# Kernel tuning notes

Measured on AMD Instinct MI355X. Metric: run time of the kernel, lower is better.

## Reference

```python
import jax, jax.numpy as jnp
import numpy as np

ROTATION_SHIFT = 15
B, L = 4096, 2048  # batch, code length


def _shift_schedule(r):
    # [0, -1, 1, -2, 2, ..., -r, r] as in the torch loop
    s = [0]
    for x in range(1, r + 1):
        s += [-x, x]
    return jnp.asarray(s, dtype=jnp.int32)


def setup_inputs() -> dict:
    key = jax.random.key(0)
    k1, k2, k3, k4 = jax.random.split(key, 4)
    shape = (2, B, L, 2)
    mk = lambda k: jax.random.randint(k, shape, 0, 2).astype(jnp.bool_)
    return {
        "iris_codes_a": mk(k1),
        "mask_codes_a": mk(k2),
        "iris_codes_b": mk(k3),
        "mask_codes_b": mk(k4),
    }


def reference(iris_codes_a, mask_codes_a, iris_codes_b, mask_codes_b):
    shifts = _shift_schedule(ROTATION_SHIFT)

    def hdist(shift):
        # roll probe codes along the code-length axis (axis=2 of (2,B,L,2))
        ia = jnp.roll(iris_codes_a, shift, axis=2)
        ma = jnp.roll(mask_codes_a, shift, axis=2)
        maskbits = ma & mask_codes_b                      # (2,B,L,2) bool
        irisbits = (ia != iris_codes_b) & maskbits        # masked non-matching bits
        # counts can exceed 2^24, so accumulate in int32 before casting
        num = jnp.sum(irisbits, dtype=jnp.int32).astype(jnp.float32)
        den = jnp.sum(maskbits, dtype=jnp.int32).astype(jnp.float32)
        return num / den

    init = jnp.minimum(jnp.ones((), jnp.float32), hdist(shifts[0]))

    def step(carry, s):
        return jnp.minimum(carry, hdist(s)), None

    match_dist, _ = jax.lax.scan(step, init, shifts[1:])
    return match_dist.reshape(1)  # torch.ones(1) makes the output shape (1,)
```

## Files before the change

### kernel.cpp

```cpp
#include <hip/hip_runtime.h>
#include <stdint.h>

typedef unsigned long long u64;
typedef unsigned int u32;

#define NACC    31
#define NSHIFT  15
#define NROWS   8192
#define ROWB    4096
#define NBLK    2048
#define NSHADOW 32

__device__ __forceinline__ void pack16(uint4 v, u32& P0, u32& P1, int t) {
    const u32 q0 = __byte_perm(v.x, v.y, 0x6420);
    const u32 q1 = __byte_perm(v.x, v.y, 0x7531);
    const u32 q2 = __byte_perm(v.z, v.w, 0x6420);
    const u32 q3 = __byte_perm(v.z, v.w, 0x7531);
    const u32 n0 = (q0 * 0x01020408u) >> 24;
    const u32 n1 = (q1 * 0x01020408u) >> 24;
    const u32 n2 = (q2 * 0x01020408u) >> 24;
    const u32 n3 = (q3 * 0x01020408u) >> 24;
    P0 |= (n0 | (n2 << 4)) << (8 * t);
    P1 |= (n1 | (n3 << 4)) << (8 * t);
}

__global__ __launch_bounds__(256) void hd_main(
    const unsigned char* __restrict__ ia, const unsigned char* __restrict__ ma,
    const unsigned char* __restrict__ ib, const unsigned char* __restrict__ mb,
    u32* __restrict__ cnt)
{
    const int tid  = threadIdx.x;
    const int lane = tid & 63;
    const int row  = blockIdx.x * 4 + (tid >> 6);

    u32 acc[NACC];
#pragma unroll
    for (int j = 0; j < NACC; ++j) acc[j] = 0u;

    const int prevL = (lane + 63) & 63;
    const int nextL = (lane + 1) & 63;

    {
        const uint4* pa = (const uint4*)(ia + (size_t)row * ROWB) + lane * 4;
        const uint4* pm = (const uint4*)(ma + (size_t)row * ROWB) + lane * 4;
        const uint4* pb = (const uint4*)(ib + (size_t)row * ROWB) + lane * 4;
        const uint4* pn = (const uint4*)(mb + (size_t)row * ROWB) + lane * 4;

        u32 A0 = 0, A1 = 0, M0 = 0, M1 = 0, B0 = 0, B1 = 0, N0 = 0, N1 = 0;
#pragma unroll
        for (int t = 0; t < 4; ++t) {
            const uint4 va = pa[t];
            const uint4 vm = pm[t];
            const uint4 vb = pb[t];
            const uint4 vn = pn[t];
            pack16(va, A0, A1, t);
            pack16(vm, M0, M1, t);
            pack16(vb, B0, B1, t);
            pack16(vn, N0, N1, t);
        }

        const u32 pA0 = __shfl(A0, prevL, 64), pA1 = __shfl(A1, prevL, 64);
        const u32 pM0 = __shfl(M0, prevL, 64), pM1 = __shfl(M1, prevL, 64);
        const u32 nA0 = __shfl(A0, nextL, 64), nA1 = __shfl(A1, nextL, 64);
        const u32 nM0 = __shfl(M0, nextL, 64), nM1 = __shfl(M1, nextL, 64);

        {
            const u32 k0 = M0 & N0, k1 = M1 & N1;
            const u32 nm = __popc((A0 ^ B0) & k0) + __popc((A1 ^ B1) & k1);
            const u32 dn = __popc(k0) + __popc(k1);
            acc[15] += nm | (dn << 16);
        }
#pragma unroll
        for (int s = 1; s <= NSHIFT; ++s) {
            {
                const u32 ra0 = (A0 << s) | (pA0 >> (32 - s));
                const u32 ra1 = (A1 << s) | (pA1 >> (32 - s));
                const u32 rm0 = (M0 << s) | (pM0 >> (32 - s));
                const u32 rm1 = (M1 << s) | (pM1 >> (32 - s));
                const u32 k0 = rm0 & N0, k1 = rm1 & N1;
                const u32 nm = __popc((ra0 ^ B0) & k0) + __popc((ra1 ^ B1) & k1);
                const u32 dn = __popc(k0) + __popc(k1);
                acc[15 + s] += nm | (dn << 16);
            }
            {
                const u32 ra0 = (A0 >> s) | (nA0 << (32 - s));
                const u32 ra1 = (A1 >> s) | (nA1 << (32 - s));
                const u32 rm0 = (M0 >> s) | (nM0 << (32 - s));
                const u32 rm1 = (M1 >> s) | (nM1 << (32 - s));
                const u32 k0 = rm0 & N0, k1 = rm1 & N1;
                const u32 nm = __popc((ra0 ^ B0) & k0) + __popc((ra1 ^ B1) & k1);
                const u32 dn = __popc(k0) + __popc(k1);
                acc[15 - s] += nm | (dn << 16);
            }
        }
    }

    __shared__ alignas(16) u32 red[NACC][264];
#pragma unroll
    for (int j = 0; j < NACC; ++j) red[j][tid] = acc[j];
    __syncthreads();

    if (tid < 248) {
        const int j = tid >> 3, c = tid & 7;
        u32 ns = 0, ds = 0;
#pragma unroll
        for (int i = 0; i < 8; ++i) {
            const uint4 v = *(const uint4*)&red[j][c * 32 + i * 4];
            ns += (v.x & 0xFFFFu) + (v.y & 0xFFFFu) + (v.z & 0xFFFFu) + (v.w & 0xFFFFu);
            ds += (v.x >> 16) + (v.y >> 16) + (v.z >> 16) + (v.w >> 16);
        }
#pragma unroll
        for (int o = 1; o < 8; o <<= 1) {
            ns += __shfl_xor(ns, o, 64);
            ds += __shfl_xor(ds, o, 64);
        }
        if (c == 0) {
            const int sh = blockIdx.x & (NSHADOW - 1);
            atomicAdd(&cnt[sh * 62 + j], ns);
            atomicAdd(&cnt[sh * 62 + 31 + j], ds);
        }
    }
}

__global__ void hd_finalize(const u32* __restrict__ cnt, float* __restrict__ out)
{
    __shared__ float fs[64];
    const int tid = threadIdx.x;
    u32 s = 0;
    if (tid < 62) {
#pragma unroll
        for (int sh = 0; sh < NSHADOW; ++sh) s += cnt[sh * 62 + tid];
    }
    fs[tid < 62 ? tid : 63] = (float)s;
    __syncthreads();
    float f = 1.0f;
    if (tid < NACC) f = fs[tid] / fs[31 + tid];
#pragma unroll
    for (int o = 32; o > 0; o >>= 1) f = fminf(f, __shfl_xor(f, o, 64));
    if (tid == 0) out[0] = fminf(f, 1.0f);
}

extern "C" void kernel_launch(void* const* d_in, const int* in_sizes, int n_in,
                              void* d_out, int out_size, void* d_ws, size_t ws_size,
                              hipStream_t stream)
{
    const unsigned char* ia = (const unsigned char*)d_in[0];
    const unsigned char* ma = (const unsigned char*)d_in[1];
    const unsigned char* ib = (const unsigned char*)d_in[2];
    const unsigned char* mb = (const unsigned char*)d_in[3];
    u32* cnt = (u32*)d_ws;

    hipMemsetAsync(d_ws, 0, NSHADOW * 62 * sizeof(u32), stream);
    hd_main<<<dim3(NBLK), dim3(256), 0, stream>>>(ia, ma, ib, mb, cnt);
    hd_finalize<<<dim3(1), dim3(64), 0, stream>>>(cnt, (float*)d_out);
}
```

Before: 35.71 us.

## Process four rows per wave with register prefetch and cheaper block reduction

Each wavefront now handles four rows, and the grid shrinks from 2048 to 512 blocks. The next row's loads are issued into registers while the current row is packed and compared. The block reduction first folds wave halves with a shuffle, which halves shared-memory traffic. The shadow counters are transposed so the finalize kernel can read them with vector loads. The aim is to hide memory latency and cut per-block overhead, at the cost of more registers and fewer blocks to spread over the CUs.

```diff
diff --git a/kernel.cpp b/kernel.cpp
--- a/kernel.cpp
+++ b/kernel.cpp
@@ -1,15 +1,14 @@
 #include <hip/hip_runtime.h>
 #include <stdint.h>
 
-typedef unsigned long long u64;
 typedef unsigned int u32;
 
-#define NACC    31
-#define NSHIFT  15
-#define NROWS   8192
-#define ROWB    4096
-#define NBLK    2048
-#define NSHADOW 32
+#define NACC   31
+#define NSHIFT 15
+#define ROWB   4096
+#define NBLK   512
+#define RPW    4
+#define NSH    32
 
 __device__ __forceinline__ void pack16(uint4 v, u32& P0, u32& P1, int t) {
     const u32 q0 = __byte_perm(v.x, v.y, 0x6420);
@@ -24,39 +23,53 @@
     P1 |= (n1 | (n3 << 4)) << (8 * t);
 }
 
-__global__ __launch_bounds__(256) void hd_main(
+__global__ __launch_bounds__(256, 2) void hd_main(
     const unsigned char* __restrict__ ia, const unsigned char* __restrict__ ma,
     const unsigned char* __restrict__ ib, const unsigned char* __restrict__ mb,
     u32* __restrict__ cnt)
 {
     const int tid  = threadIdx.x;
     const int lane = tid & 63;
-    const int row  = blockIdx.x * 4 + (tid >> 6);
+    const int wv   = tid >> 6;
+    const int gw   = blockIdx.x * 4 + wv;
+
+    const int prevL = (lane + 63) & 63;
+    const int nextL = (lane + 1) & 63;
 
     u32 acc[NACC];
 #pragma unroll
     for (int j = 0; j < NACC; ++j) acc[j] = 0u;
 
-    const int prevL = (lane + 63) & 63;
-    const int nextL = (lane + 1) & 63;
+    const uint4* pa = (const uint4*)(ia + (size_t)gw * RPW * ROWB) + lane * 4;
+    const uint4* pm = (const uint4*)(ma + (size_t)gw * RPW * ROWB) + lane * 4;
+    const uint4* pb = (const uint4*)(ib + (size_t)gw * RPW * ROWB) + lane * 4;
+    const uint4* pn = (const uint4*)(mb + (size_t)gw * RPW * ROWB) + lane * 4;
+    const int rstep = ROWB / 16;
 
-    {
-        const uint4* pa = (const uint4*)(ia + (size_t)row * ROWB) + lane * 4;
-        const uint4* pm = (const uint4*)(ma + (size_t)row * ROWB) + lane * 4;
-        const uint4* pb = (const uint4*)(ib + (size_t)row * ROWB) + lane * 4;
-        const uint4* pn = (const uint4*)(mb + (size_t)row * ROWB) + lane * 4;
+    uint4 bA[4], bM[4], bB[4], bN[4];
+#pragma unroll
+    for (int t = 0; t < 4; ++t) {
+        bA[t] = pa[t]; bM[t] = pm[t]; bB[t] = pb[t]; bN[t] = pn[t];
+    }
 
+#pragma unroll
+    for (int r = 0; r < RPW; ++r) {
         u32 A0 = 0, A1 = 0, M0 = 0, M1 = 0, B0 = 0, B1 = 0, N0 = 0, N1 = 0;
 #pragma unroll
         for (int t = 0; t < 4; ++t) {
-            const uint4 va = pa[t];
-            const uint4 vm = pm[t];
-            const uint4 vb = pb[t];
-            const uint4 vn = pn[t];
-            pack16(va, A0, A1, t);
-            pack16(vm, M0, M1, t);
-            pack16(vb, B0, B1, t);
-            pack16(vn, N0, N1, t);
+            pack16(bA[t], A0, A1, t);
+            pack16(bM[t], M0, M1, t);
+            pack16(bB[t], B0, B1, t);
+            pack16(bN[t], N0, N1, t);
+        }
+
+        if (r + 1 < RPW) {
+            const int o = (r + 1) * rstep;
+#pragma unroll
+            for (int t = 0; t < 4; ++t) {
+                bA[t] = pa[o + t]; bM[t] = pm[o + t];
+                bB[t] = pb[o + t]; bN[t] = pn[o + t];
+            }
         }
 
         const u32 pA0 = __shfl(A0, prevL, 64), pA1 = __shfl(A1, prevL, 64);
@@ -95,49 +108,58 @@
         }
     }
 
-    __shared__ alignas(16) u32 red[NACC][264];
+    __shared__ alignas(16) u32 red[32][132];
 #pragma unroll
-    for (int j = 0; j < NACC; ++j) red[j][tid] = acc[j];
+    for (int j = 0; j < NACC; ++j) acc[j] += __shfl_xor(acc[j], 32, 64);
+#pragma unroll
+    for (int j = 0; j < NACC; j += 2) {
+        const u32 v = (j + 1 < NACC && (lane & 32)) ? acc[j + 1] : acc[j];
+        red[j + (lane >> 5)][wv * 32 + (lane & 31)] = v;
+    }
     __syncthreads();
 
     if (tid < 248) {
         const int j = tid >> 3, c = tid & 7;
-        u32 ns = 0, ds = 0;
+        const uint4* p = (const uint4*)&red[j][c * 16];
+        u32 sn = 0, sd = 0;
 #pragma unroll
-        for (int i = 0; i < 8; ++i) {
-            const uint4 v = *(const uint4*)&red[j][c * 32 + i * 4];
-            ns += (v.x & 0xFFFFu) + (v.y & 0xFFFFu) + (v.z & 0xFFFFu) + (v.w & 0xFFFFu);
-            ds += (v.x >> 16) + (v.y >> 16) + (v.z >> 16) + (v.w >> 16);
+        for (int i = 0; i < 4; ++i) {
+            const uint4 v = p[i];
+            sn += (v.x & 0xFFFFu) + (v.y & 0xFFFFu) + (v.z & 0xFFFFu) + (v.w & 0xFFFFu);
+            sd += (v.x >> 16) + (v.y >> 16) + (v.z >> 16) + (v.w >> 16);
         }
-#pragma unroll
-        for (int o = 1; o < 8; o <<= 1) {
-            ns += __shfl_xor(ns, o, 64);
-            ds += __shfl_xor(ds, o, 64);
-        }
+        sn += __shfl_xor(sn, 1, 64); sd += __shfl_xor(sd, 1, 64);
+        sn += __shfl_xor(sn, 2, 64); sd += __shfl_xor(sd, 2, 64);
+        sn += __shfl_xor(sn, 4, 64); sd += __shfl_xor(sd, 4, 64);
         if (c == 0) {
-            const int sh = blockIdx.x & (NSHADOW - 1);
-            atomicAdd(&cnt[sh * 62 + j], ns);
-            atomicAdd(&cnt[sh * 62 + 31 + j], ds);
+            const int sh = blockIdx.x & (NSH - 1);
+            atomicAdd(&cnt[j * NSH + sh], sn);
+            atomicAdd(&cnt[(31 + j) * NSH + sh], sd);
         }
     }
 }
 
 __global__ void hd_finalize(const u32* __restrict__ cnt, float* __restrict__ out)
 {
-    __shared__ float fs[64];
+    __shared__ u32 gathered[62];
     const int tid = threadIdx.x;
-    u32 s = 0;
-    if (tid < 62) {
+    if (tid < 248) {
+        const int j = tid >> 2, q = tid & 3;
+        const uint4* p = (const uint4*)&cnt[j * NSH + q * 8];
+        const uint4 v0 = p[0], v1 = p[1];
+        u32 s = v0.x + v0.y + v0.z + v0.w + v1.x + v1.y + v1.z + v1.w;
+        s += __shfl_xor(s, 1, 64);
+        s += __shfl_xor(s, 2, 64);
+        if (q == 0) gathered[j] = s;
+    }
+    __syncthreads();
+    if (tid < 64) {
+        float f = 1.0f;
+        if (tid < NACC) f = (float)gathered[tid] / (float)gathered[31 + tid];
 #pragma unroll
-        for (int sh = 0; sh < NSHADOW; ++sh) s += cnt[sh * 62 + tid];
+        for (int o = 32; o > 0; o >>= 1) f = fminf(f, __shfl_xor(f, o, 64));
+        if (tid == 0) out[0] = fminf(f, 1.0f);
     }
-    fs[tid < 62 ? tid : 63] = (float)s;
-    __syncthreads();
-    float f = 1.0f;
-    if (tid < NACC) f = fs[tid] / fs[31 + tid];
-#pragma unroll
-    for (int o = 32; o > 0; o >>= 1) f = fminf(f, __shfl_xor(f, o, 64));
-    if (tid == 0) out[0] = fminf(f, 1.0f);
 }
 
 extern "C" void kernel_launch(void* const* d_in, const int* in_sizes, int n_in,
@@ -150,7 +172,7 @@
     const unsigned char* mb = (const unsigned char*)d_in[3];
     u32* cnt = (u32*)d_ws;
 
-    hipMemsetAsync(d_ws, 0, NSHADOW * 62 * sizeof(u32), stream);
+    hipMemsetAsync(d_ws, 0, 62 * NSH * sizeof(u32), stream);
     hd_main<<<dim3(NBLK), dim3(256), 0, stream>>>(ia, ma, ib, mb, cnt);
-    hd_finalize<<<dim3(1), dim3(64), 0, stream>>>(cnt, (float*)d_out);
+    hd_finalize<<<dim3(1), dim3(256), 0, stream>>>(cnt, (float*)d_out);
 }
```

New measurement: 40.25 us. 12.7% more time.
